# Performance work log

Measured on AMD Instinct MI355X. Metric: run time of the kernel, lower is better.

## Reference

```python
import jax, jax.numpy as jnp
import numpy as np
import math

N, C, E, K_TOP = 4096, 256, 131072, 32
NEG_SLOPE = 0.2  # GATConv default negative_slope


def _mlp(x, w1, b1, w2, b2):
    # Linear -> relu -> Linear (dropout is identity in eval mode)
    return jax.nn.relu(x @ w1 + b1) @ w2 + b2


def _gat_alpha(x, w, a_src, a_dst, src, dst, n):
    # PyG GATConv attention coefficients (heads=1), softmax over incoming edges per dst
    h = x @ w                                                   # [N,C]
    logits = jax.nn.leaky_relu((h @ a_src)[src] + (h @ a_dst)[dst], NEG_SLOPE)  # [E]
    m = jnp.full((n,), -jnp.inf, dtype=logits.dtype).at[dst].max(logits)
    e = jnp.exp(logits - m[dst])
    s = jax.ops.segment_sum(e, dst, num_segments=n)
    return e / s[dst]                                           # [E]


def _mha_w(x, wq, bq, wk, bk):
    # nn.MultiheadAttention attention weights, heads=1, unbatched [N,C] input
    q = x @ wq + bq
    k = x @ wk + bk
    return jax.nn.softmax((q @ k.T) * (1.0 / math.sqrt(C)), axis=-1)  # [N,N]


def _forward(ae, pe, se,
             ae_w1, ae_b1, ae_w2, ae_b2,
             pe_w1, pe_b1, pe_w2, pe_b2,
             se_w1, se_b1, se_w2, se_b2,
             ae_gw, ae_as, ae_ad,
             pe_gw, pe_as, pe_ad,
             se_gw, se_as, se_ad,
             ae_wq, ae_bq, ae_wk, ae_bk,
             pe_wq, pe_bq, pe_wk, pe_bk,
             se_wq, se_bq, se_wk, se_bk,
             a_l, b_l, c_l, a_g, b_g, c_g,
             w_local, w_global,
             edge_index, K):
    n = ae.shape[0]
    ae = _mlp(ae, ae_w1, ae_b1, ae_w2, ae_b2)
    pe = _mlp(pe, pe_w1, pe_b1, pe_w2, pe_b2)
    se = _mlp(se, se_w1, se_b1, se_w2, se_b2)

    src, dst = edge_index[0], edge_index[1]

    # ---- local branch: fused GAT attention coeffs -> weighted mean aggregation ----
    pa = _gat_alpha(pe, pe_gw, pe_as, pe_ad, src, dst, n)
    sa = _gat_alpha(se, se_gw, se_as, se_ad, src, dst, n)
    aa = _gat_alpha(ae, ae_gw, ae_as, ae_ad, src, dst, n)
    local_attn = a_l * pa + b_l * sa + c_l * aa                 # [E]
    msg = local_attn[:, None] * ae[src]                         # [E,C]
    summ = jax.ops.segment_sum(msg, dst, num_segments=n)
    cnt = jax.ops.segment_sum(jnp.ones((src.shape[0],), msg.dtype), dst, num_segments=n)
    out_local = summ / jnp.maximum(cnt, 1.0)[:, None]           # mean aggr

    # ---- global branch: dense self-attn maps + adj masking + per-column top-K ----
    pw = _mha_w(pe, pe_wq, pe_bq, pe_wk, pe_bk)                 # [N,N]
    sw = _mha_w(se, se_wq, se_bq, se_wk, se_bk)
    aw = _mha_w(ae, ae_wq, ae_bq, ae_wk, ae_bk)
    sample_attn = a_g * pw + b_g * sw
    adj = jnp.zeros((n, n), sample_attn.dtype).at[src, dst].add(1.0)
    sample_attn = jnp.where(adj > 0, jnp.zeros((), sample_attn.dtype), sample_attn)
    # torch topk(dim=1) on [1,N,N] == top-K along axis 0 (per column) of [N,N]
    _, idx = jax.lax.top_k(sample_attn.T, K)                    # [N,K] row indices per column
    maskT = jnp.zeros((n, n), sample_attn.dtype).at[jnp.arange(n)[:, None], idx].set(1.0)
    mask = maskT.T
    g_attn = (0.5 * a_g + 0.5 * b_g) * (sample_attn * mask) + c_g * (aw * mask)
    col = jnp.sum(g_attn, axis=0)                               # column sums (torch dim=1 on [1,N,N])
    g_attn = g_attn / col[None, :]
    out_global = g_attn @ ae                                    # [N,C]

    return out_local @ w_local + out_global @ w_global


def setup_inputs() -> dict:
    key = jax.random.key(0)
    it = iter(jax.random.split(key, 64))
    g = lambda shape, s=0.06: jax.random.normal(next(it), shape, dtype=jnp.float32) * s
    inp = {"ae": g((N, C), 1.0), "pe": g((N, C), 1.0), "se": g((N, C), 1.0)}
    for p in ("ae", "pe", "se"):
        inp[p + "_w1"] = g((C, 2 * C)); inp[p + "_b1"] = jnp.zeros((2 * C,), jnp.float32)
        inp[p + "_w2"] = g((2 * C, C)); inp[p + "_b2"] = jnp.zeros((C,), jnp.float32)
        inp[p + "_gw"] = g((C, C)); inp[p + "_as"] = g((C,)); inp[p + "_ad"] = g((C,))
        inp[p + "_wq"] = g((C, C)); inp[p + "_bq"] = jnp.zeros((C,), jnp.float32)
        inp[p + "_wk"] = g((C, C)); inp[p + "_bk"] = jnp.zeros((C,), jnp.float32)
    for s in ("a_l", "b_l", "c_l", "a_g", "b_g", "c_g"):
        inp[s] = jnp.float32(0.33)
    inp["w_local"] = g((C, C))
    inp["w_global"] = g((C, C))
    inp["edge_index"] = jax.random.randint(next(it), (2, E), 0, N, dtype=jnp.int32)
    inp["K"] = K_TOP
    return inp


def reference(ae, pe, se,
              ae_w1, ae_b1, ae_w2, ae_b2,
              pe_w1, pe_b1, pe_w2, pe_b2,
              se_w1, se_b1, se_w2, se_b2,
              ae_gw, ae_as, ae_ad,
              pe_gw, pe_as, pe_ad,
              se_gw, se_as, se_ad,
              ae_wq, ae_bq, ae_wk, ae_bk,
              pe_wq, pe_bq, pe_wk, pe_bk,
              se_wq, se_bq, se_wk, se_bk,
              a_l, b_l, c_l, a_g, b_g, c_g,
              w_local, w_global,
              edge_index, K):
    return _forward(ae, pe, se,
                    ae_w1, ae_b1, ae_w2, ae_b2,
                    pe_w1, pe_b1, pe_w2, pe_b2,
                    se_w1, se_b1, se_w2, se_b2,
                    ae_gw, ae_as, ae_ad,
                    pe_gw, pe_as, pe_ad,
                    se_gw, se_as, se_ad,
                    ae_wq, ae_bq, ae_wk, ae_bk,
                    pe_wq, pe_bq, pe_wk, pe_bk,
                    se_wq, se_bq, se_wk, se_bk,
                    a_l, b_l, c_l, a_g, b_g, c_g,
                    w_local, w_global,
                    edge_index, K)
```

## Files before the change

### kernel.cpp

```cpp
#include <hip/hip_runtime.h>

#define NN 4096
#define CC 256
#define EE 131072
#define KT 32

typedef unsigned short ushort_t;
typedef __attribute__((ext_vector_type(8))) short short8;
typedef __attribute__((ext_vector_type(4))) float float4v;

__device__ __forceinline__ ushort_t f2bf(float x) {
    union { float f; unsigned u; } a; a.f = x;
    unsigned r = (a.u + 0x7FFF + ((a.u >> 16) & 1)) >> 16;
    return (ushort_t)r;
}
__device__ __forceinline__ float bf2f(ushort_t b) {
    union { float f; unsigned u; } a; a.u = ((unsigned)b) << 16;
    return a.f;
}
__device__ __forceinline__ float fexp(float x) {
#if __has_builtin(__builtin_amdgcn_exp2f)
    return __builtin_amdgcn_exp2f(x * 1.4426950408889634f);
#else
    return exp2f(x * 1.4426950408889634f);
#endif
}

constexpr size_t OFF_EPT  = 0;
constexpr size_t OFF_EST  = OFF_EPT + 16777216;
constexpr size_t OFF_LP   = OFF_EST + 16777216;
constexpr size_t OFF_LS   = OFF_LP + 4096;
constexpr size_t OFF_LA   = OFF_LS + 4096;
constexpr size_t OFF_ECNT = OFF_LA + 4096;
constexpr size_t OFF_GCNT = OFF_ECNT + 4096;
constexpr size_t OFF_ADJ  = OFF_GCNT + 4096;
constexpr size_t ZERO_END = OFF_ADJ + 524288;
constexpr size_t OFF_XM   = ZERO_END;
constexpr size_t OFF_QK   = OFF_XM + 3*1048576;
constexpr size_t OFF_WEXP = OFF_QK + 6*1048576;
constexpr size_t OFF_HS   = OFF_WEXP + 3*131072;
constexpr size_t OFF_HD   = OFF_HS + 12288;
constexpr size_t OFF_WSD  = OFF_HD + 12288;
constexpr size_t OFF_TKI  = OFF_WSD + 1536;
constexpr size_t OFF_TKV  = OFF_TKI + 131072;
constexpr size_t OFF_GN   = OFF_TKV + 131072;
constexpr size_t OFF_EOFF = OFF_GN + 131072;
constexpr size_t OFF_ECUR = OFF_EOFF + 4097;
constexpr size_t OFF_ELST = OFF_ECUR + 4096;
constexpr size_t OFF_GOFF = OFF_ELST + 131072;
constexpr size_t OFF_GCUR = OFF_GOFF + 4097;
constexpr size_t OFF_GLST = OFF_GCUR + 4096;
constexpr size_t OFF_WLT  = OFF_GLST + 131072;
constexpr size_t WS_FLOATS = OFF_WLT + 131072;

constexpr size_t SH_XINH = 0;
constexpr size_t SH_XINL = 3145728;
constexpr size_t SH_HIDH = 6291456;
constexpr size_t SH_HIDL = 12582912;
constexpr size_t SH_XMH  = 18874368;
constexpr size_t SH_XML  = 22020096;
constexpr size_t SH_WT   = 25165824;
constexpr size_t WT_BR   = 786432;

struct TArgs {
    const float* s[14]; ushort_t* h[14]; ushort_t* l[14];
    int nshift[14]; int total[14]; int kstride[14]; int koff[14];
};

__global__ __launch_bounds__(256)
void wtrans_k(TArgs a)
{
    int z = blockIdx.z;
    int idx = blockIdx.x * 256 + threadIdx.x;
    if (idx >= a.total[z]) return;
    int n = idx & ((1 << a.nshift[z]) - 1);
    int k = idx >> a.nshift[z];
    float v = a.s[z][idx];
    ushort_t hh = f2bf(v);
    size_t o = (size_t)n * a.kstride[z] + a.koff[z] + k;
    a.h[z][o] = hh;
    a.l[z][o] = f2bf(v - bf2f(hh));
}

__global__ __launch_bounds__(256)
void split3_k(const float* s0, const float* s1, const float* s2,
              ushort_t* hb, ushort_t* lb, size_t nper)
{
    int z = blockIdx.z;
    const float* s = (z == 0) ? s0 : (z == 1) ? s1 : s2;
    ushort_t* h = hb + (size_t)z * nper;
    ushort_t* l = lb + (size_t)z * nper;
    size_t i = (size_t)(blockIdx.x * 256 + threadIdx.x) * 4;
    float4 v = *(const float4*)(s + i);
    ushort_t h0 = f2bf(v.x), h1 = f2bf(v.y), h2 = f2bf(v.z), h3 = f2bf(v.w);
    ushort_t l0 = f2bf(v.x - bf2f(h0)), l1 = f2bf(v.y - bf2f(h1));
    ushort_t l2 = f2bf(v.z - bf2f(h2)), l3 = f2bf(v.w - bf2f(h3));
    uint2 hw, lw;
    hw.x = (unsigned)h0 | ((unsigned)h1 << 16); hw.y = (unsigned)h2 | ((unsigned)h3 << 16);
    lw.x = (unsigned)l0 | ((unsigned)l1 << 16); lw.y = (unsigned)l2 | ((unsigned)l3 << 16);
    *(uint2*)(h + i) = hw;
    *(uint2*)(l + i) = lw;
}

struct MArgs {
    const ushort_t* Ah[6]; const ushort_t* Al[6];
    const ushort_t* Bh[6]; const ushort_t* Bl[6];
    const float* bias[6];
    float* Cf[6]; ushort_t* Ch[6]; ushort_t* Cl[6];
};

template<int RELU>
__global__ __launch_bounds__(256)
void mgemm_k(MArgs a, int N, int K)
{
    __shared__ ushort_t SA[2][128 * 32];
    __shared__ ushort_t SB[2][64 * 32];

    const int z = blockIdx.z;
    const int t = threadIdx.x, wave = t >> 6, lane = t & 63;
    const int lrow = lane & 15, lquad = lane >> 4;

    const ushort_t* src = (wave == 0) ? a.Ah[z] : (wave == 1) ? a.Al[z]
                        : (wave == 2) ? a.Bh[z] : a.Bl[z];
    ushort_t* dst = (wave == 0) ? &SA[0][0] : (wave == 1) ? &SA[1][0]
                  : (wave == 2) ? &SB[0][0] : &SB[1][0];
    const int rbase = (wave < 2) ? blockIdx.x * 128 : blockIdx.y * 64;
    const int sr = lane >> 2, sq = lane & 3;
    const int gsq = sq ^ ((sr >> 1) & 3);

    float4v acc[2][4] = {};

    for (int k0 = 0; k0 < K; k0 += 32) {
        if (wave < 2) {
            #pragma unroll
            for (int it = 0; it < 8; ++it) {
                const ushort_t* g = src + (size_t)(rbase + it * 16 + sr) * K + k0 + gsq * 8;
                __builtin_amdgcn_global_load_lds(
                    (const __attribute__((address_space(1))) void*)g,
                    (__attribute__((address_space(3))) void*)(dst + it * 512),
                    16, 0, 0);
            }
        } else {
            #pragma unroll
            for (int it = 0; it < 4; ++it) {
                const ushort_t* g = src + (size_t)(rbase + it * 16 + sr) * K + k0 + gsq * 8;
                __builtin_amdgcn_global_load_lds(
                    (const __attribute__((address_space(1))) void*)g,
                    (__attribute__((address_space(3))) void*)(dst + it * 512),
                    16, 0, 0);
            }
        }
        __syncthreads();

        short8 fAh[2], fAl[2], fBh[4], fBl[4];
        #pragma unroll
        for (int mt = 0; mt < 2; ++mt) {
            int ra = wave * 32 + mt * 16 + lrow;
            int ca = (lquad ^ ((ra >> 1) & 3)) * 8;
            fAh[mt] = *(const short8*)&SA[0][ra * 32 + ca];
            fAl[mt] = *(const short8*)&SA[1][ra * 32 + ca];
        }
        #pragma unroll
        for (int nt = 0; nt < 4; ++nt) {
            int rb = nt * 16 + lrow;
            int cb = (lquad ^ ((rb >> 1) & 3)) * 8;
            fBh[nt] = *(const short8*)&SB[0][rb * 32 + cb];
            fBl[nt] = *(const short8*)&SB[1][rb * 32 + cb];
        }
        #pragma unroll
        for (int mt = 0; mt < 2; ++mt)
            #pragma unroll
            for (int nt = 0; nt < 4; ++nt) {
                acc[mt][nt] = __builtin_amdgcn_mfma_f32_16x16x32_bf16(fAh[mt], fBh[nt], acc[mt][nt], 0, 0, 0);
                acc[mt][nt] = __builtin_amdgcn_mfma_f32_16x16x32_bf16(fAh[mt], fBl[nt], acc[mt][nt], 0, 0, 0);
                acc[mt][nt] = __builtin_amdgcn_mfma_f32_16x16x32_bf16(fAl[mt], fBh[nt], acc[mt][nt], 0, 0, 0);
            }
        __syncthreads();
    }

    const float* bias = a.bias[z];
    float* Cf = a.Cf[z];
    ushort_t* Ch = a.Ch[z]; ushort_t* Cl = a.Cl[z];
    const int i0w = blockIdx.x * 128 + wave * 32, j0w = blockIdx.y * 64;
    #pragma unroll
    for (int mt = 0; mt < 2; ++mt) {
        const int ib = i0w + mt * 16 + lquad * 4;
        #pragma unroll
        for (int nt = 0; nt < 4; ++nt) {
            const int j = j0w + nt * 16 + lrow;
            float bj = bias ? bias[j] : 0.f;
            #pragma unroll
            for (int r = 0; r < 4; ++r) {
                float v = acc[mt][nt][r] + bj;
                if (RELU) v = fmaxf(v, 0.f);
                if (Cf) Cf[(size_t)(ib + r) * N + j] = v;
                if (Ch) {
                    ushort_t h = f2bf(v);
                    Ch[(size_t)(ib + r) * N + j] = h;
                    Cl[(size_t)(ib + r) * N + j] = f2bf(v - bf2f(h));
                }
            }
        }
    }
}

struct QArgs {
    const ushort_t* qh[3]; const ushort_t* ql[3];
    const ushort_t* kh[3]; const ushort_t* kl[3];
    float* ept[3]; float* rs[3];
};

__global__ __launch_bounds__(256)
void qk_mfma_k(QArgs a, float scale)
{
    __shared__ ushort_t SA[2][128 * 32];
    __shared__ ushort_t SB[2][128 * 32];

    const int z = blockIdx.z;
    const int t = threadIdx.x;
    const int wave = t >> 6, lane = t & 63;
    const int wi = wave & 1, wj = wave >> 1;
    const int i0w = blockIdx.x * 128 + wi * 64;
    const int j0w = blockIdx.y * 128 + wj * 64;
    const int lrow = lane & 15, lquad = lane >> 4;

    const ushort_t* src = (wave == 0) ? a.qh[z] : (wave == 1) ? a.ql[z]
                        : (wave == 2) ? a.kh[z] : a.kl[z];
    ushort_t* dst = (wave == 0) ? &SA[0][0] : (wave == 1) ? &SA[1][0]
                  : (wave == 2) ? &SB[0][0] : &SB[1][0];
    const int rbase = (wave < 2) ? blockIdx.x * 128 : blockIdx.y * 128;
    const int sr = lane >> 2, sq = lane & 3;
    const int gsq = sq ^ ((sr >> 1) & 3);

    float4v acc[4][4] = {};

    for (int k0 = 0; k0 < CC; k0 += 32) {
        #pragma unroll
        for (int it = 0; it < 8; ++it) {
            const ushort_t* g = src + (size_t)(rbase + it * 16 + sr) * CC + k0 + gsq * 8;
            __builtin_amdgcn_global_load_lds(
                (const __attribute__((address_space(1))) void*)g,
                (__attribute__((address_space(3))) void*)(dst + it * 512),
                16, 0, 0);
        }
        __syncthreads();

        short8 Ah[4], Al[4], Bh[4], Bl[4];
        #pragma unroll
        for (int mt = 0; mt < 4; ++mt) {
            int ra = wi * 64 + mt * 16 + lrow;
            int ca = (lquad ^ ((ra >> 1) & 3)) * 8;
            Ah[mt] = *(const short8*)&SA[0][ra * 32 + ca];
            Al[mt] = *(const short8*)&SA[1][ra * 32 + ca];
        }
        #pragma unroll
        for (int nt = 0; nt < 4; ++nt) {
            int rb = wj * 64 + nt * 16 + lrow;
            int cb = (lquad ^ ((rb >> 1) & 3)) * 8;
            Bh[nt] = *(const short8*)&SB[0][rb * 32 + cb];
            Bl[nt] = *(const short8*)&SB[1][rb * 32 + cb];
        }
        #pragma unroll
        for (int mt = 0; mt < 4; ++mt)
            #pragma unroll
            for (int nt = 0; nt < 4; ++nt) {
                acc[mt][nt] = __builtin_amdgcn_mfma_f32_16x16x32_bf16(Ah[mt], Bh[nt], acc[mt][nt], 0, 0, 0);
                acc[mt][nt] = __builtin_amdgcn_mfma_f32_16x16x32_bf16(Ah[mt], Bl[nt], acc[mt][nt], 0, 0, 0);
                acc[mt][nt] = __builtin_amdgcn_mfma_f32_16x16x32_bf16(Al[mt], Bh[nt], acc[mt][nt], 0, 0, 0);
            }
        __syncthreads();
    }

    float* ept = a.ept[z];
    float* rowsum = a.rs[z];
    #pragma unroll
    for (int mt = 0; mt < 4; ++mt) {
        const int ib = i0w + mt * 16 + lquad * 4;
        float part[4] = {0.f, 0.f, 0.f, 0.f};
        #pragma unroll
        for (int nt = 0; nt < 4; ++nt) {
            const int j = j0w + nt * 16 + lrow;
            float e0 = fexp(acc[mt][nt][0] * scale);
            float e1 = fexp(acc[mt][nt][1] * scale);
            float e2 = fexp(acc[mt][nt][2] * scale);
            float e3 = fexp(acc[mt][nt][3] * scale);
            part[0] += e0; part[1] += e1; part[2] += e2; part[3] += e3;
            if (ept)
                *(float4*)&ept[(size_t)j * NN + ib] = make_float4(e0, e1, e2, e3);
        }
        #pragma unroll
        for (int r = 0; r < 4; ++r) {
            float p = part[r];
            p += __shfl_xor(p, 1, 64);
            p += __shfl_xor(p, 2, 64);
            p += __shfl_xor(p, 4, 64);
            p += __shfl_xor(p, 8, 64);
            if (lrow == 0) atomicAdd(&rowsum[ib + r], p);
        }
    }
}

__global__ void invrows_k(float* __restrict__ lp, float* __restrict__ ls,
                          const float* agp, const float* bgp)
{
    int i = blockIdx.x * 256 + threadIdx.x;
    lp[i] = (*agp) / lp[i];
    ls[i] = (*bgp) / ls[i];
}

__global__ __launch_bounds__(256)
void gatvec_k(const float* g0, const float* g1, const float* g2,
              const float* v0, const float* v1, const float* v2,
              const float* v3, const float* v4, const float* v5,
              float* __restrict__ wsd)
{
    int b = blockIdx.x;
    const float* gw = (b < 2) ? g0 : (b < 4) ? g1 : g2;
    const float* av = (b == 0) ? v0 : (b == 1) ? v1 : (b == 2) ? v2
                    : (b == 3) ? v3 : (b == 4) ? v4 : v5;
    int tdx = threadIdx.x;
    float s = 0.f;
    for (int c = 0; c < CC; ++c) s += gw[(size_t)tdx * CC + c] * av[c];
    wsd[b * 256 + tdx] = s;
}

__global__ __launch_bounds__(256)
void hshd_k(const float* __restrict__ Xp, const float* __restrict__ Xs,
            const float* __restrict__ Xa, const float* __restrict__ wsd,
            float* __restrict__ hs, float* __restrict__ hd)
{
    int b = blockIdx.y, row = blockIdx.x, t = threadIdx.x;
    const float* X = (b == 0) ? Xp : (b == 1) ? Xs : Xa;
    float x = X[(size_t)row * CC + t];
    float p1 = x * wsd[b * 512 + t];
    float p2 = x * wsd[b * 512 + 256 + t];
    for (int off = 32; off; off >>= 1) {
        p1 += __shfl_down(p1, off, 64);
        p2 += __shfl_down(p2, off, 64);
    }
    __shared__ float s1[4], s2[4];
    if ((t & 63) == 0) { s1[t >> 6] = p1; s2[t >> 6] = p2; }
    __syncthreads();
    if (t == 0) {
        hs[b * NN + row] = s1[0] + s1[1] + s1[2] + s1[3];
        hd[b * NN + row] = s2[0] + s2[1] + s2[2] + s2[3];
    }
}

__global__ __launch_bounds__(256)
void edge_k(const int* __restrict__ ei, const float* __restrict__ hs,
            const float* __restrict__ hd, float* __restrict__ wexp,
            unsigned* __restrict__ bits, int* __restrict__ cnt)
{
    int e = blockIdx.x * 256 + threadIdx.x;
    int s = ei[e], d = ei[EE + e];
    #pragma unroll
    for (int b = 0; b < 3; ++b) {
        float l = hs[b * NN + s] + hd[b * NN + d];
        l = (l > 0.f) ? l : 0.2f * l;
        wexp[(size_t)b * EE + e] = fexp(l);
    }
    size_t lin = (size_t)d * NN + s;
    atomicOr(&bits[lin >> 5], 1u << (lin & 31));
    atomicAdd(&cnt[d], 1);
}

__global__ void gcount_k(const int* __restrict__ tki, int* __restrict__ cnt)
{
    int p = blockIdx.x * 256 + threadIdx.x;
    atomicAdd(&cnt[tki[p]], 1);
}

__global__ __launch_bounds__(256)
void prefix_k(const int* __restrict__ cnt, int* __restrict__ off, int* __restrict__ cur)
{
    __shared__ int part[257];
    int t = threadIdx.x;
    int loc[16]; int s = 0;
    #pragma unroll
    for (int u = 0; u < 16; ++u) { loc[u] = s; s += cnt[t * 16 + u]; }
    part[t + 1] = s;
    if (t == 0) part[0] = 0;
    __syncthreads();
    if (t == 0) for (int i = 1; i <= 256; ++i) part[i] += part[i - 1];
    __syncthreads();
    int b = part[t];
    #pragma unroll
    for (int u = 0; u < 16; ++u) { off[t * 16 + u] = b + loc[u]; cur[t * 16 + u] = b + loc[u]; }
    if (t == 255) off[4096] = part[256];
}

__global__ void efill_k(const int* __restrict__ ei, int* __restrict__ cur,
                        int* __restrict__ lst)
{
    int e = blockIdx.x * 256 + threadIdx.x;
    int p = atomicAdd(&cur[ei[EE + e]], 1);
    lst[p] = e;
}

__global__ void gfill_k(const int* __restrict__ tki, int* __restrict__ cur,
                        int* __restrict__ lst)
{
    int p = blockIdx.x * 256 + threadIdx.x;
    int q = atomicAdd(&cur[tki[p]], 1);
    lst[q] = p;
}

__global__ __launch_bounds__(256)
void topk_k(const float* __restrict__ EPT, const float* __restrict__ EST,
            const float* __restrict__ ivp, const float* __restrict__ ivs,
            const unsigned* __restrict__ adjbits,
            int* __restrict__ tki, float* __restrict__ tkv)
{
    __shared__ unsigned lv[4][KT];
    __shared__ int      li[4][KT];
    const int j = blockIdx.x, t = threadIdx.x;
    const int w = t >> 6, lane = t & 63;
    const size_t base = (size_t)j * NN;

    unsigned keys[16], kmax = 0;
    #pragma unroll
    for (int u = 0; u < 16; ++u) {
        int i = w * 1024 + u * 64 + lane;
        float v = EPT[base + i] * ivp[i] + EST[base + i] * ivs[i];
        if ((adjbits[(base + i) >> 5] >> (i & 31)) & 1u) v = 0.f;
        union { float f; unsigned u32; } cv; cv.f = v;
        keys[u] = (cv.u32 & 0xFFFFFFF0u) | (unsigned)(15 - u);
        kmax = keys[u] > kmax ? keys[u] : kmax;
    }

    for (int r = 0; r < KT; ++r) {
        unsigned k = kmax;
        #pragma unroll
        for (int off = 1; off < 64; off <<= 1) {
            unsigned o = __shfl_xor(k, off, 64);
            k = o > k ? o : k;
        }
        if (lane == 0) lv[w][r] = k;
        if (kmax == k) {
            int u_win = 15 - (int)(k & 0xFu);
            li[w][r] = w * 1024 + u_win * 64 + lane;
            kmax = 0;
            #pragma unroll
            for (int u = 0; u < 16; ++u) {
                if (keys[u] == k) keys[u] = 0;
                kmax = keys[u] > kmax ? keys[u] : kmax;
            }
        }
    }
    __syncthreads();

    if (t == 0) {
        unsigned hv[4] = {lv[0][0], lv[1][0], lv[2][0], lv[3][0]};
        int      hi_[4] = {li[0][0], li[1][0], li[2][0], li[3][0]};
        int      pp[4] = {0, 0, 0, 0};
        for (int r = 0; r < KT; ++r) {
            int best = 0;
            #pragma unroll
            for (int wsel = 1; wsel < 4; ++wsel)
                if (hv[wsel] > hv[best] || (hv[wsel] == hv[best] && hi_[wsel] < hi_[best]))
                    best = wsel;
            union { unsigned u32; float f; } cv; cv.u32 = hv[best] & 0xFFFFFFF0u;
            tkv[j * KT + r] = cv.f;
            tki[j * KT + r] = hi_[best];
            int p = ++pp[best];
            hv[best]  = (p < KT) ? lv[best][p] : 0u;
            hi_[best] = (p < KT) ? li[best][p] : 0x7FFFFFFF;
        }
    }
}

__global__ __launch_bounds__(256)
void awcol_k(const ushort_t* __restrict__ qh, const ushort_t* __restrict__ ql,
             const ushort_t* __restrict__ kh, const ushort_t* __restrict__ kl,
             const float* __restrict__ La, const int* __restrict__ tki,
             const float* __restrict__ tkv,
             const float* agp, const float* bgp, const float* cgp,
             float* __restrict__ gn)
{
    __shared__ float kj[CC];
    __shared__ float gv[KT];
    __shared__ float cs_sh;
    int j = blockIdx.x, t = threadIdx.x;
    kj[t] = bf2f(kh[(size_t)j * CC + t]) + bf2f(kl[(size_t)j * CC + t]);
    __syncthreads();
    float hg = 0.5f * (*agp) + 0.5f * (*bgp), cg = *cgp;
    int wv = t >> 6, ln = t & 63;
    for (int k = wv; k < KT; k += 4) {
        int i = tki[j * KT + k];
        float p = 0.f;
        #pragma unroll
        for (int u = 0; u < 4; ++u) {
            int c = ln + u * 64;
            float q = bf2f(qh[(size_t)i * CC + c]) + bf2f(ql[(size_t)i * CC + c]);
            p += q * kj[c];
        }
        for (int off = 32; off; off >>= 1) p += __shfl_down(p, off, 64);
        if (ln == 0) {
            float aw = fexp(p * 0.0625f) / La[i];
            gv[k] = hg * tkv[j * KT + k] + cg * aw;
        }
    }
    __syncthreads();
    if (t == 0) { float cs = 0.f; for (int k = 0; k < KT; ++k) cs += gv[k]; cs_sh = cs; }
    __syncthreads();
    if (t < KT) gn[j * KT + t] = gv[t] / cs_sh;
}

__device__ __forceinline__ void gather_accum(const float* __restrict__ aem, int ln, int n,
                                             float la, int s, float4& acc)
{
    int u = 0;
    for (; u + 4 <= n; u += 4) {
        float l0 = __shfl(la, u, 64),     l1 = __shfl(la, u + 1, 64);
        float l2 = __shfl(la, u + 2, 64), l3 = __shfl(la, u + 3, 64);
        int   s0 = __shfl(s, u, 64),      s1 = __shfl(s, u + 1, 64);
        int   s2 = __shfl(s, u + 2, 64),  s3 = __shfl(s, u + 3, 64);
        const float4 v0 = *(const float4*)&aem[(size_t)s0 * CC + ln * 4];
        const float4 v1 = *(const float4*)&aem[(size_t)s1 * CC + ln * 4];
        const float4 v2 = *(const float4*)&aem[(size_t)s2 * CC + ln * 4];
        const float4 v3 = *(const float4*)&aem[(size_t)s3 * CC + ln * 4];
        acc.x += l0 * v0.x + l1 * v1.x + l2 * v2.x + l3 * v3.x;
        acc.y += l0 * v0.y + l1 * v1.y + l2 * v2.y + l3 * v3.y;
        acc.z += l0 * v0.z + l1 * v1.z + l2 * v2.z + l3 * v3.z;
        acc.w += l0 * v0.w + l1 * v1.w + l2 * v2.w + l3 * v3.w;
    }
    for (; u < n; ++u) {
        float lu = __shfl(la, u, 64);
        int   su = __shfl(s, u, 64);
        const float4 v = *(const float4*)&aem[(size_t)su * CC + ln * 4];
        acc.x += lu * v.x; acc.y += lu * v.y;
        acc.z += lu * v.z; acc.w += lu * v.w;
    }
}

__global__ __launch_bounds__(256)
void gather_k(const int* __restrict__ ei, const int* __restrict__ eoff,
              const int* __restrict__ elst, const float* __restrict__ wexp,
              const int* __restrict__ goff, const int* __restrict__ glst,
              const float* __restrict__ gn, const float* __restrict__ aem,
              const float* alp, const float* blp, const float* clp,
              ushort_t* __restrict__ outch, ushort_t* __restrict__ outcl)
{
    int wv = threadIdx.x >> 6, ln = threadIdx.x & 63;
    float4 acc = {0.f, 0.f, 0.f, 0.f};

    if (blockIdx.x < NN / 4) {
        int d = blockIdx.x * 4 + wv;
        int beg = eoff[d], end = eoff[d + 1];

        float s1 = 0.f, s2 = 0.f, s3 = 0.f;
        for (int c = beg + ln; c < end; c += 64) {
            int e = elst[c];
            s1 += wexp[e];
            s2 += wexp[EE + e];
            s3 += wexp[2 * (size_t)EE + e];
        }
        #pragma unroll
        for (int off = 1; off < 64; off <<= 1) {
            s1 += __shfl_xor(s1, off, 64);
            s2 += __shfl_xor(s2, off, 64);
            s3 += __shfl_xor(s3, off, 64);
        }
        float i0 = (*alp) / s1, i1 = (*blp) / s2, i2 = (*clp) / s3;

        for (int c = beg; c < end; c += 64) {
            int n = min(64, end - c);
            int s = 0; float la = 0.f;
            if (ln < n) {
                int e = elst[c + ln];
                s = ei[e];
                la = i0 * wexp[e] + i1 * wexp[EE + e] + i2 * wexp[2 * (size_t)EE + e];
            }
            gather_accum(aem, ln, n, la, s, acc);
        }
        float inv = 1.f / fmaxf((float)(end - beg), 1.f);
        acc.x *= inv; acc.y *= inv; acc.z *= inv; acc.w *= inv;

        ushort_t h0 = f2bf(acc.x), h1 = f2bf(acc.y), h2 = f2bf(acc.z), h3 = f2bf(acc.w);
        uint2 hw, lw;
        hw.x = (unsigned)h0 | ((unsigned)h1 << 16); hw.y = (unsigned)h2 | ((unsigned)h3 << 16);
        lw.x = (unsigned)f2bf(acc.x - bf2f(h0)) | ((unsigned)f2bf(acc.y - bf2f(h1)) << 16);
        lw.y = (unsigned)f2bf(acc.z - bf2f(h2)) | ((unsigned)f2bf(acc.w - bf2f(h3)) << 16);
        *(uint2*)&outch[(size_t)d * 512 + ln * 4] = hw;
        *(uint2*)&outcl[(size_t)d * 512 + ln * 4] = lw;
    } else {
        int i = (blockIdx.x - NN / 4) * 4 + wv;
        int beg = goff[i], end = goff[i + 1];
        for (int c = beg; c < end; c += 64) {
            int n = min(64, end - c);
            int jcol = 0; float g = 0.f;
            if (ln < n) {
                int p = glst[c + ln];
                jcol = p >> 5;
                g = gn[p];
            }
            gather_accum(aem, ln, n, g, jcol, acc);
        }
        ushort_t h0 = f2bf(acc.x), h1 = f2bf(acc.y), h2 = f2bf(acc.z), h3 = f2bf(acc.w);
        uint2 hw, lw;
        hw.x = (unsigned)h0 | ((unsigned)h1 << 16); hw.y = (unsigned)h2 | ((unsigned)h3 << 16);
        lw.x = (unsigned)f2bf(acc.x - bf2f(h0)) | ((unsigned)f2bf(acc.y - bf2f(h1)) << 16);
        lw.y = (unsigned)f2bf(acc.z - bf2f(h2)) | ((unsigned)f2bf(acc.w - bf2f(h3)) << 16);
        *(uint2*)&outch[(size_t)i * 512 + 256 + ln * 4] = hw;
        *(uint2*)&outcl[(size_t)i * 512 + 256 + ln * 4] = lw;
    }
}

__global__ void diag_k(float* out, float v) { out[0] = v; }

extern "C" void kernel_launch(void* const* d_in, const int* in_sizes, int n_in,
                              void* d_out, int out_size, void* d_ws, size_t ws_size,
                              hipStream_t stream)
{
    (void)in_sizes; (void)n_in; (void)out_size;

    if (ws_size < WS_FLOATS * sizeof(float)) {
        diag_k<<<1, 1, 0, stream>>>((float*)d_out, (float)(ws_size >> 20));
        return;
    }

    float* W = (float*)d_ws;
    float* EPT = W + OFF_EPT;  float* EST = W + OFF_EST;
    float* LP = W + OFF_LP;    float* LS = W + OFF_LS;   float* LA = W + OFF_LA;
    int* ECNT = (int*)(W + OFF_ECNT);
    int* GCNT = (int*)(W + OFF_GCNT);
    unsigned* ADJ = (unsigned*)(W + OFF_ADJ);
    float* XM = W + OFF_XM;
    ushort_t* QKS = (ushort_t*)(W + OFF_QK);
    float* WEXP = W + OFF_WEXP;
    float* HS = W + OFF_HS;    float* HD = W + OFF_HD;   float* WSD = W + OFF_WSD;
    int*   TKI = (int*)(W + OFF_TKI);
    float* TKV = W + OFF_TKV;  float* GN = W + OFF_GN;
    int* EOFF = (int*)(W + OFF_EOFF); int* ECUR = (int*)(W + OFF_ECUR);
    int* ELST = (int*)(W + OFF_ELST);
    int* GOFF = (int*)(W + OFF_GOFF); int* GCUR = (int*)(W + OFF_GCUR);
    int* GLST = (int*)(W + OFF_GLST);

    ushort_t* PRO = (ushort_t*)EPT;
    ushort_t* EPI = (ushort_t*)EST;
    ushort_t* WLT = (ushort_t*)(W + OFF_WLT);

    ushort_t* XINH = PRO + SH_XINH; ushort_t* XINL = PRO + SH_XINL;
    ushort_t* HIDH = PRO + SH_HIDH; ushort_t* HIDL = PRO + SH_HIDL;
    ushort_t* XMH  = PRO + SH_XMH;  ushort_t* XML  = PRO + SH_XML;

    auto W1T = [&](int b, int hl) { return PRO + SH_WT + (size_t)b * WT_BR + hl * 131072; };
    auto W2T = [&](int b, int hl) { return PRO + SH_WT + (size_t)b * WT_BR + 262144 + hl * 131072; };
    auto WQT = [&](int b, int hl) { return PRO + SH_WT + (size_t)b * WT_BR + 524288 + hl * 65536; };
    auto WKT = [&](int b, int hl) { return PRO + SH_WT + (size_t)b * WT_BR + 655360 + hl * 65536; };
    ushort_t* WCT_H = WLT;
    ushort_t* WCT_L = WLT + 131072;
    ushort_t* OUTCH = EPI;
    ushort_t* OUTCL = EPI + 2097152;

    auto QHp = [&](int b) { return QKS + (size_t)(b * 4 + 0) * 1048576; };
    auto QLp = [&](int b) { return QKS + (size_t)(b * 4 + 1) * 1048576; };
    auto KHp = [&](int b) { return QKS + (size_t)(b * 4 + 2) * 1048576; };
    auto KLp = [&](int b) { return QKS + (size_t)(b * 4 + 3) * 1048576; };

    const float* Xin[3] = {(const float*)d_in[1], (const float*)d_in[2], (const float*)d_in[0]};
    const int base_idx[3] = {14, 25, 3};
    const float *w1[3], *b1[3], *w2[3], *b2[3], *gw[3], *asv[3], *adv[3], *wq[3], *bq[3], *wk[3], *bk[3];
    for (int b = 0; b < 3; ++b) {
        int o = base_idx[b];
        w1[b] = (const float*)d_in[o + 0]; b1[b] = (const float*)d_in[o + 1];
        w2[b] = (const float*)d_in[o + 2]; b2[b] = (const float*)d_in[o + 3];
        gw[b] = (const float*)d_in[o + 4]; asv[b] = (const float*)d_in[o + 5];
        adv[b] = (const float*)d_in[o + 6];
        wq[b] = (const float*)d_in[o + 7]; bq[b] = (const float*)d_in[o + 8];
        wk[b] = (const float*)d_in[o + 9]; bk[b] = (const float*)d_in[o + 10];
    }
    const float* al = (const float*)d_in[36]; const float* bl = (const float*)d_in[37];
    const float* cl = (const float*)d_in[38];
    const float* ag = (const float*)d_in[39]; const float* bg = (const float*)d_in[40];
    const float* cg = (const float*)d_in[41];
    const float* wloc = (const float*)d_in[42];
    const float* wglb = (const float*)d_in[43];
    const int* ei = (const int*)d_in[44];

    dim3 blk(256);

    hipMemsetAsync(LP, 0, (ZERO_END - OFF_LP) * sizeof(float), stream);

    {
        TArgs a{};
        for (int b = 0; b < 3; ++b) {
            a.s[b] = w1[b]; a.h[b] = W1T(b, 0); a.l[b] = W1T(b, 1);
            a.nshift[b] = 9; a.total[b] = 131072; a.kstride[b] = 256; a.koff[b] = 0;
            a.s[3 + b] = w2[b]; a.h[3 + b] = W2T(b, 0); a.l[3 + b] = W2T(b, 1);
            a.nshift[3 + b] = 8; a.total[3 + b] = 131072; a.kstride[3 + b] = 512; a.koff[3 + b] = 0;
            a.s[6 + b] = wq[b]; a.h[6 + b] = WQT(b, 0); a.l[6 + b] = WQT(b, 1);
            a.nshift[6 + b] = 8; a.total[6 + b] = 65536; a.kstride[6 + b] = 256; a.koff[6 + b] = 0;
            a.s[9 + b] = wk[b]; a.h[9 + b] = WKT(b, 0); a.l[9 + b] = WKT(b, 1);
            a.nshift[9 + b] = 8; a.total[9 + b] = 65536; a.kstride[9 + b] = 256; a.koff[9 + b] = 0;
        }
        a.s[12] = wloc; a.h[12] = WCT_H; a.l[12] = WCT_L;
        a.nshift[12] = 8; a.total[12] = 65536; a.kstride[12] = 512; a.koff[12] = 0;
        a.s[13] = wglb; a.h[13] = WCT_H; a.l[13] = WCT_L;
        a.nshift[13] = 8; a.total[13] = 65536; a.kstride[13] = 512; a.koff[13] = 256;
        wtrans_k<<<dim3(512, 1, 14), blk, 0, stream>>>(a);
    }

    split3_k<<<dim3(1024, 1, 3), blk, 0, stream>>>(Xin[0], Xin[1], Xin[2], XINH, XINL, 1048576);

    {
        MArgs a{};
        for (int b = 0; b < 3; ++b) {
            a.Ah[b] = XINH + (size_t)b * 1048576; a.Al[b] = XINL + (size_t)b * 1048576;
            a.Bh[b] = W1T(b, 0); a.Bl[b] = W1T(b, 1); a.bias[b] = b1[b];
            a.Cf[b] = nullptr;
            a.Ch[b] = HIDH + (size_t)b * 2097152; a.Cl[b] = HIDL + (size_t)b * 2097152;
        }
        mgemm_k<1><<<dim3(32, 8, 3), blk, 0, stream>>>(a, 512, 256);
    }
    {
        MArgs a{};
        for (int b = 0; b < 3; ++b) {
            a.Ah[b] = HIDH + (size_t)b * 2097152; a.Al[b] = HIDL + (size_t)b * 2097152;
            a.Bh[b] = W2T(b, 0); a.Bl[b] = W2T(b, 1); a.bias[b] = b2[b];
            a.Cf[b] = XM + (size_t)b * 1048576;
            a.Ch[b] = XMH + (size_t)b * 1048576; a.Cl[b] = XML + (size_t)b * 1048576;
        }
        mgemm_k<0><<<dim3(32, 4, 3), blk, 0, stream>>>(a, 256, 512);
    }

    gatvec_k<<<6, blk, 0, stream>>>(gw[0], gw[1], gw[2],
                                    asv[0], adv[0], asv[1], adv[1], asv[2], adv[2], WSD);
    hshd_k<<<dim3(NN, 3), blk, 0, stream>>>(XM, XM + 1048576, XM + 2 * 1048576, WSD, HS, HD);
    edge_k<<<EE / 256, blk, 0, stream>>>(ei, HS, HD, WEXP, ADJ, ECNT);

    prefix_k<<<1, blk, 0, stream>>>(ECNT, EOFF, ECUR);
    efill_k<<<EE / 256, blk, 0, stream>>>(ei, ECUR, ELST);

    {
        MArgs a{};
        for (int b = 0; b < 3; ++b) {
            a.Ah[b] = XMH + (size_t)b * 1048576; a.Al[b] = XML + (size_t)b * 1048576;
            a.Bh[b] = WQT(b, 0); a.Bl[b] = WQT(b, 1); a.bias[b] = bq[b];
            a.Cf[b] = nullptr; a.Ch[b] = QHp(b); a.Cl[b] = QLp(b);
            a.Ah[3 + b] = a.Ah[b]; a.Al[3 + b] = a.Al[b];
            a.Bh[3 + b] = WKT(b, 0); a.Bl[3 + b] = WKT(b, 1); a.bias[3 + b] = bk[b];
            a.Cf[3 + b] = nullptr; a.Ch[3 + b] = KHp(b); a.Cl[3 + b] = KLp(b);
        }
        mgemm_k<0><<<dim3(32, 4, 6), blk, 0, stream>>>(a, 256, 256);
    }

    {
        QArgs a{};
        for (int b = 0; b < 3; ++b) {
            a.qh[b] = QHp(b); a.ql[b] = QLp(b); a.kh[b] = KHp(b); a.kl[b] = KLp(b);
        }
        a.ept[0] = EPT; a.rs[0] = LP;
        a.ept[1] = EST; a.rs[1] = LS;
        a.ept[2] = nullptr; a.rs[2] = LA;
        qk_mfma_k<<<dim3(32, 32, 3), blk, 0, stream>>>(a, 0.0625f);
    }

    invrows_k<<<16, blk, 0, stream>>>(LP, LS, ag, bg);

    topk_k<<<NN, blk, 0, stream>>>(EPT, EST, LP, LS, ADJ, TKI, TKV);

    gcount_k<<<(NN * KT) / 256, blk, 0, stream>>>(TKI, GCNT);
    prefix_k<<<1, blk, 0, stream>>>(GCNT, GOFF, GCUR);
    gfill_k<<<(NN * KT) / 256, blk, 0, stream>>>(TKI, GCUR, GLST);

    awcol_k<<<NN, blk, 0, stream>>>(QHp(2), QLp(2), KHp(2), KLp(2), LA,
                                    TKI, TKV, ag, bg, cg, GN);

    gather_k<<<NN / 2, blk, 0, stream>>>(ei, EOFF, ELST, WEXP, GOFF, GLST, GN,
                                         XM + 2 * 1048576, al, bl, cl, OUTCH, OUTCL);

    {
        MArgs a{};
        a.Ah[0] = OUTCH; a.Al[0] = OUTCL;
        a.Bh[0] = WCT_H; a.Bl[0] = WCT_L; a.bias[0] = nullptr;
        a.Cf[0] = (float*)d_out; a.Ch[0] = nullptr; a.Cl[0] = nullptr;
        mgemm_k<0><<<dim3(32, 4, 1), blk, 0, stream>>>(a, 256, 512);
    }
}
```

Baseline: 554.1 us.

## Fuse top-k count/fill into neighbors, cache top-4 per lane, shuffle-scan prefix

Removes the separate gcount and gfill kernel launches. The count atomics move into the end of topk_k and the list fill moves into the start of awcol_k. The per-lane top-k selection now keeps a sorted top-4 cache, so it only rescans its 16 keys once every four wins instead of after every win. The single-thread serial prefix in prefix_k becomes a wavefront shuffle scan. The trade-off is extra register pressure in topk_k, a small amount of extra work in awcol_k, and a dependence on GLST ordering being produced by atomics inside awcol_k.

```diff
diff --git a/kernel.cpp b/kernel.cpp
--- a/kernel.cpp
+++ b/kernel.cpp
@@ -365,29 +365,32 @@
     atomicAdd(&cnt[d], 1);
 }
 
-__global__ void gcount_k(const int* __restrict__ tki, int* __restrict__ cnt)
-{
-    int p = blockIdx.x * 256 + threadIdx.x;
-    atomicAdd(&cnt[tki[p]], 1);
-}
-
 __global__ __launch_bounds__(256)
 void prefix_k(const int* __restrict__ cnt, int* __restrict__ off, int* __restrict__ cur)
 {
-    __shared__ int part[257];
-    int t = threadIdx.x;
+    __shared__ int wsum[4];
+    int t = threadIdx.x, lane = t & 63, w = t >> 6;
     int loc[16]; int s = 0;
     #pragma unroll
     for (int u = 0; u < 16; ++u) { loc[u] = s; s += cnt[t * 16 + u]; }
-    part[t + 1] = s;
-    if (t == 0) part[0] = 0;
+    int v = s;
+    #pragma unroll
+    for (int d = 1; d < 64; d <<= 1) {
+        int o = __shfl_up(v, d, 64);
+        if (lane >= d) v += o;
+    }
+    if (lane == 63) wsum[w] = v;
     __syncthreads();
-    if (t == 0) for (int i = 1; i <= 256; ++i) part[i] += part[i - 1];
-    __syncthreads();
-    int b = part[t];
+    int base = 0;
     #pragma unroll
-    for (int u = 0; u < 16; ++u) { off[t * 16 + u] = b + loc[u]; cur[t * 16 + u] = b + loc[u]; }
-    if (t == 255) off[4096] = part[256];
+    for (int x = 0; x < 3; ++x) base += (x < w) ? wsum[x] : 0;
+    int excl = base + v - s;
+    #pragma unroll
+    for (int u = 0; u < 16; ++u) {
+        off[t * 16 + u] = excl + loc[u];
+        cur[t * 16 + u] = excl + loc[u];
+    }
+    if (t == 255) off[4096] = base + v;
 }
 
 __global__ void efill_k(const int* __restrict__ ei, int* __restrict__ cur,
@@ -398,19 +401,12 @@
     lst[p] = e;
 }
 
-__global__ void gfill_k(const int* __restrict__ tki, int* __restrict__ cur,
-                        int* __restrict__ lst)
-{
-    int p = blockIdx.x * 256 + threadIdx.x;
-    int q = atomicAdd(&cur[tki[p]], 1);
-    lst[q] = p;
-}
-
 __global__ __launch_bounds__(256)
 void topk_k(const float* __restrict__ EPT, const float* __restrict__ EST,
             const float* __restrict__ ivp, const float* __restrict__ ivs,
             const unsigned* __restrict__ adjbits,
-            int* __restrict__ tki, float* __restrict__ tkv)
+            int* __restrict__ tki, float* __restrict__ tkv,
+            int* __restrict__ gcnt)
 {
     __shared__ unsigned lv[4][KT];
     __shared__ int      li[4][KT];
@@ -418,33 +414,47 @@
     const int w = t >> 6, lane = t & 63;
     const size_t base = (size_t)j * NN;
 
-    unsigned keys[16], kmax = 0;
+    unsigned keys[16];
+    unsigned m0 = 0, m1 = 0, m2 = 0, m3 = 0;
     #pragma unroll
     for (int u = 0; u < 16; ++u) {
         int i = w * 1024 + u * 64 + lane;
         float v = EPT[base + i] * ivp[i] + EST[base + i] * ivs[i];
         if ((adjbits[(base + i) >> 5] >> (i & 31)) & 1u) v = 0.f;
         union { float f; unsigned u32; } cv; cv.f = v;
-        keys[u] = (cv.u32 & 0xFFFFFFF0u) | (unsigned)(15 - u);
-        kmax = keys[u] > kmax ? keys[u] : kmax;
-    }
-
+        unsigned k = (cv.u32 & 0xFFFFFFF0u) | (unsigned)(15 - u);
+        keys[u] = k;
+        bool g0 = k > m0, g1 = k > m1, g2 = k > m2, g3 = k > m3;
+        m3 = g3 ? (g2 ? m2 : k) : m3;
+        m2 = g2 ? (g1 ? m1 : k) : m2;
+        m1 = g1 ? (g0 ? m0 : k) : m1;
+        m0 = g0 ? k : m0;
+    }
+
+    unsigned consumed = 0;
     for (int r = 0; r < KT; ++r) {
-        unsigned k = kmax;
+        unsigned k = m0;
         #pragma unroll
         for (int off = 1; off < 64; off <<= 1) {
             unsigned o = __shfl_xor(k, off, 64);
             k = o > k ? o : k;
         }
         if (lane == 0) lv[w][r] = k;
-        if (kmax == k) {
+        if (m0 == k) {
             int u_win = 15 - (int)(k & 0xFu);
             li[w][r] = w * 1024 + u_win * 64 + lane;
-            kmax = 0;
-            #pragma unroll
-            for (int u = 0; u < 16; ++u) {
-                if (keys[u] == k) keys[u] = 0;
-                kmax = keys[u] > kmax ? keys[u] : kmax;
+            consumed |= (1u << u_win);
+            m0 = m1; m1 = m2; m2 = m3; m3 = 0;
+            if (m0 == 0) {
+                #pragma unroll
+                for (int u = 0; u < 16; ++u) {
+                    unsigned kk = ((consumed >> u) & 1u) ? 0u : keys[u];
+                    bool g0 = kk > m0, g1 = kk > m1, g2 = kk > m2, g3 = kk > m3;
+                    m3 = g3 ? (g2 ? m2 : kk) : m3;
+                    m2 = g2 ? (g1 ? m1 : kk) : m2;
+                    m1 = g1 ? (g0 ? m0 : kk) : m1;
+                    m0 = g0 ? kk : m0;
+                }
             }
         }
     }
@@ -468,6 +478,9 @@
             hi_[best] = (p < KT) ? li[best][p] : 0x7FFFFFFF;
         }
     }
+    __syncthreads();
+
+    if (t < KT) atomicAdd(&gcnt[tki[j * KT + t]], 1);
 }
 
 __global__ __launch_bounds__(256)
@@ -476,12 +489,20 @@
              const float* __restrict__ La, const int* __restrict__ tki,
              const float* __restrict__ tkv,
              const float* agp, const float* bgp, const float* cgp,
-             float* __restrict__ gn)
+             float* __restrict__ gn,
+             int* __restrict__ gcur, int* __restrict__ glst)
 {
     __shared__ float kj[CC];
     __shared__ float gv[KT];
     __shared__ float cs_sh;
     int j = blockIdx.x, t = threadIdx.x;
+
+    if (t < KT) {
+        int p = j * KT + t;
+        int q = atomicAdd(&gcur[tki[p]], 1);
+        glst[q] = p;
+    }
+
     kj[t] = bf2f(kh[(size_t)j * CC + t]) + bf2f(kl[(size_t)j * CC + t]);
     __syncthreads();
     float hg = 0.5f * (*agp) + 0.5f * (*bgp), cg = *cgp;
@@ -759,14 +780,12 @@
 
     invrows_k<<<16, blk, 0, stream>>>(LP, LS, ag, bg);
 
-    topk_k<<<NN, blk, 0, stream>>>(EPT, EST, LP, LS, ADJ, TKI, TKV);
-
-    gcount_k<<<(NN * KT) / 256, blk, 0, stream>>>(TKI, GCNT);
+    topk_k<<<NN, blk, 0, stream>>>(EPT, EST, LP, LS, ADJ, TKI, TKV, GCNT);
+
     prefix_k<<<1, blk, 0, stream>>>(GCNT, GOFF, GCUR);
-    gfill_k<<<(NN * KT) / 256, blk, 0, stream>>>(TKI, GCUR, GLST);
 
     awcol_k<<<NN, blk, 0, stream>>>(QHp(2), QLp(2), KHp(2), KLp(2), LA,
-                                    TKI, TKV, ag, bg, cg, GN);
+                                    TKI, TKV, ag, bg, cg, GN, GCUR, GLST);
 
     gather_k<<<NN / 2, blk, 0, stream>>>(ei, EOFF, ELST, WEXP, GOFF, GLST, GN,
                                          XM + 2 * 1048576, al, bl, cl, OUTCH, OUTCL);
```

Result: faster. 529.9 us (-4.4%).
